# Kernel tuning notes

Hardware: AMD Instinct MI355X
Metric: run time of the kernel (lower is better)

The kernel has to match this reference:

```python
import jax, jax.numpy as jnp
import numpy as np

BATCH = 8192
DIM = 256
TEMP = 0.001
EPS = 1e-12  # torch F.normalize eps


def setup_inputs() -> dict:
    key = jax.random.key(0)
    k1, k2 = jax.random.split(key)
    proj_1 = jax.random.normal(k1, (BATCH, DIM), dtype=jnp.float32)
    proj_2 = jax.random.normal(k2, (BATCH, DIM), dtype=jnp.float32)
    return {"proj_1": proj_1, "proj_2": proj_2}


def _l2_normalize(x):
    norm = jnp.maximum(jnp.linalg.norm(x, axis=1, keepdims=True), EPS)
    return x / norm


def reference(proj_1, proj_2):
    # L2-normalize rows (SimCLR z_i, z_j)
    z_i = _l2_normalize(proj_1)  # [B, D]
    z_j = _l2_normalize(proj_2)  # [B, D]
    # cosine similarity of unit vectors == dot product -> single matmul
    sim = jnp.einsum("id,jd->ij", z_i, z_j)  # [B, B]
    positives = jnp.diagonal(sim)  # [B]
    n = positives / TEMP
    all_losses = -n + jax.scipy.special.logsumexp(sim / TEMP, axis=1)
    loss = jnp.sum(all_losses) / BATCH
    return (loss, jnp.sum(positives))
```

## Files before the change

### kernel.cpp

```cpp
#include <hip/hip_runtime.h>
#include <hip/hip_fp8.h>
#include <stdint.h>
#include <stddef.h>

#define BATCH 8192
#define DIM   256

#define LN2F 0.6931471805599453f
#define SCALE_ZJ 16.0f
#define SCALE_ZI 90.16844005556021f

typedef int   v8i    __attribute__((ext_vector_type(8)));
typedef float f32x16 __attribute__((ext_vector_type(16)));


static __device__ __forceinline__ uint8_t f2fp8(float f) {
  __hip_fp8_e4m3 q(f);
  return *reinterpret_cast<uint8_t*>(&q);
}

static __device__ __forceinline__ void stage8(const uint8_t* __restrict__ src,
                                              uint8_t* dst, int tid) {
#pragma unroll
  for (int it = 0; it < 2; ++it) {
    const int off = it * 4096 + tid * 16;
    __builtin_amdgcn_global_load_lds(
        (const __attribute__((address_space(1))) void*)(src + off),
        (__attribute__((address_space(3))) void*)(dst + off),
        16, 0, 0);
  }
}

__global__ __launch_bounds__(256) void prep_kernel(
    const float* __restrict__ p1, const float* __restrict__ p2,
    uint8_t* __restrict__ Zi8, uint8_t* __restrict__ Zj8,
    float* __restrict__ pos) {
  const int lane = threadIdx.x & 63;
  const int w    = threadIdx.x >> 6;
  const int row  = blockIdx.x * 4 + w;

  const float4 x1 = ((const float4*)p1)[row * 64 + lane];
  const float4 x2 = ((const float4*)p2)[row * 64 + lane];
  float ss1 = x1.x * x1.x + x1.y * x1.y + x1.z * x1.z + x1.w * x1.w;
  float ss2 = x2.x * x2.x + x2.y * x2.y + x2.z * x2.z + x2.w * x2.w;
  float d   = x1.x * x2.x + x1.y * x2.y + x1.z * x2.z + x1.w * x2.w;
#pragma unroll
  for (int m = 1; m < 64; m <<= 1) {
    ss1 += __shfl_xor(ss1, m);
    ss2 += __shfl_xor(ss2, m);
    d   += __shfl_xor(d, m);
  }
  const float n1 = fmaxf(sqrtf(ss1), 1e-12f);
  const float n2 = fmaxf(sqrtf(ss2), 1e-12f);
  if (lane == 0) pos[row] = d / (n1 * n2);

  const float sI = SCALE_ZI / n1;
  const float sJ = SCALE_ZJ / n2;
  uchar4 u1, u2;
  u1.x = f2fp8(x1.x * sI); u1.y = f2fp8(x1.y * sI);
  u1.z = f2fp8(x1.z * sI); u1.w = f2fp8(x1.w * sI);
  u2.x = f2fp8(x2.x * sJ); u2.y = f2fp8(x2.y * sJ);
  u2.z = f2fp8(x2.z * sJ); u2.w = f2fp8(x2.w * sJ);

  const size_t tb = (size_t)(row >> 5) * 8192;
  const int off = (lane >> 4) * 2048 + ((lane >> 2) & 1) * 1024 +
                  (((lane >> 3) & 1) * 32 + (row & 31)) * 16 + (lane & 3) * 4;
  *(uchar4*)(Zi8 + tb + off) = u1;
  *(uchar4*)(Zj8 + tb + off) = u2;
}

static __device__ __forceinline__ void lse_update(const f32x16& acc,
                                                  float& m, float& l) {
  float t0 = fmaxf(fmaxf(acc[0],  acc[1]),  acc[2]);
  float t1 = fmaxf(fmaxf(acc[3],  acc[4]),  acc[5]);
  float t2 = fmaxf(fmaxf(acc[6],  acc[7]),  acc[8]);
  float t3 = fmaxf(fmaxf(acc[9],  acc[10]), acc[11]);
  t0 = fmaxf(fmaxf(t0, t1), fmaxf(fmaxf(acc[12], acc[13]), acc[14]));
  t2 = fmaxf(fmaxf(t2, t3), acc[15]);
  const float mn = fmaxf(m, fmaxf(t0, t2));
  float s0 = 0.f, s1 = 0.f;
#pragma unroll
  for (int r = 0; r < 16; r += 2) {
    s0 += __builtin_amdgcn_exp2f(acc[r + 0] - mn);
    s1 += __builtin_amdgcn_exp2f(acc[r + 1] - mn);
  }
  l = l * __builtin_amdgcn_exp2f(m - mn) + (s0 + s1);
  m = mn;
}

__global__ __launch_bounds__(256, 3) void lse_kernel(
    const uint8_t* __restrict__ Zi8, const uint8_t* __restrict__ Zj8,
    float* __restrict__ plse) {
  const int bid   = blockIdx.x;
  const int chunk = bid & 31;
  const int rb    = bid >> 5;
  const int tid   = threadIdx.x;
  const int lane  = tid & 63;
  const int w     = tid >> 6;
  const int r32   = lane & 31;
  const int h     = lane >> 5;
  const int iBase = rb * 256 + w * 64;

  __shared__ __align__(16) uint8_t lds[4][8192];

  v8i b0[4], b1[4];
  const uint8_t* zb = Zi8 + (size_t)(rb * 8 + w * 2) * 8192 + lane * 16;
#pragma unroll
  for (int q = 0; q < 4; ++q) {
    union { int4 i4[2]; v8i v; } u0, u1;
    u0.i4[0] = *(const int4*)(zb + q * 2048);
    u0.i4[1] = *(const int4*)(zb + q * 2048 + 1024);
    u1.i4[0] = *(const int4*)(zb + 8192 + q * 2048);
    u1.i4[1] = *(const int4*)(zb + 8192 + q * 2048 + 1024);
    b0[q] = u0.v; b1[q] = u1.v;
  }
#pragma unroll
  for (int q = 0; q < 4; ++q) { asm("" : "+v"(b0[q])); asm("" : "+v"(b1[q])); }

  float m0 = -1e30f, l0 = 0.f, m1 = -1e30f, l1 = 0.f;

  const uint8_t* src = Zj8 + (size_t)chunk * (8 * 8192);

  stage8(src, &lds[0][0], tid);
  stage8(src + 8192, &lds[1][0], tid);

  for (int s = 0; s < 4; ++s) {
    __syncthreads();
    if (s < 3) {
      stage8(src + (size_t)(2 * s + 2) * 8192, &lds[(2 * s + 2) & 3][0], tid);
      stage8(src + (size_t)(2 * s + 3) * 8192, &lds[(2 * s + 3) & 3][0], tid);
    }
#pragma unroll
    for (int sub = 0; sub < 2; ++sub) {
      const uint8_t* buf = &lds[(2 * s + sub) & 3][0] + lane * 16;
      f32x16 acc0 = {}, acc1 = {};
      __builtin_amdgcn_s_setprio(1);
#pragma unroll
      for (int q = 0; q < 4; ++q) {
        union { int4 i4[2]; v8i v; } ua;
        ua.i4[0] = *(const int4*)(buf + q * 2048);
        ua.i4[1] = *(const int4*)(buf + q * 2048 + 1024);
        acc0 = __builtin_amdgcn_mfma_scale_f32_32x32x64_f8f6f4(
            ua.v, b0[q], acc0, 0, 0, 0, 0x7F7F7F7F, 0, 0x7F7F7F7F);
        acc1 = __builtin_amdgcn_mfma_scale_f32_32x32x64_f8f6f4(
            ua.v, b1[q], acc1, 0, 0, 0, 0x7F7F7F7F, 0, 0x7F7F7F7F);
      }
      __builtin_amdgcn_s_setprio(0);
      lse_update(acc0, m0, l0);
      lse_update(acc1, m1, l1);
    }
  }

#pragma unroll
  for (int p = 0; p < 2; ++p) {
    float m = p ? m1 : m0;
    float l = p ? l1 : l0;
    const float mo = __shfl_xor(m, 32);
    const float lo = __shfl_xor(l, 32);
    const float mn = fmaxf(m, mo);
    l = l * __builtin_amdgcn_exp2f(m - mn) + lo * __builtin_amdgcn_exp2f(mo - mn);
    if (h == 0) {
      const int i = iBase + p * 32 + r32;
      plse[(size_t)i * 32 + chunk] = mn + __builtin_amdgcn_logf(l);
    }
  }
}

__global__ __launch_bounds__(256) void finalize_kernel(
    const float* __restrict__ plse, const float* __restrict__ pos,
    float2* __restrict__ bpart, unsigned int* __restrict__ counter,
    float* __restrict__ out) {
  const int tid = threadIdx.x;
  const int row = blockIdx.x * 256 + tid;
  float v[32];
#pragma unroll
  for (int c = 0; c < 8; ++c) {
    const float4 q = ((const float4*)(plse + (size_t)row * 32))[c];
    v[c * 4 + 0] = q.x; v[c * 4 + 1] = q.y; v[c * 4 + 2] = q.z; v[c * 4 + 3] = q.w;
  }
  float M = v[0];
#pragma unroll
  for (int c = 1; c < 32; ++c) M = fmaxf(M, v[c]);
  float S = 0.0f;
#pragma unroll
  for (int c = 0; c < 32; ++c) S += __builtin_amdgcn_exp2f(v[c] - M);
  const float lse = LN2F * (M + __builtin_amdgcn_logf(S));
  const float pv  = pos[row];
  float lsum = lse - 1000.0f * pv;
  float psum = pv;
#pragma unroll
  for (int msk = 1; msk < 64; msk <<= 1) {
    lsum += __shfl_xor(lsum, msk);
    psum += __shfl_xor(psum, msk);
  }
  __shared__ float sl[4], sp[4];
  const int w = tid >> 6, lane = tid & 63;
  if (lane == 0) { sl[w] = lsum; sp[w] = psum; }
  __syncthreads();
  if (tid == 0) {
    union { float2 f; unsigned long long u; } pk;
    pk.f = make_float2(sl[0] + sl[1] + sl[2] + sl[3],
                       sp[0] + sp[1] + sp[2] + sp[3]);
    __hip_atomic_store((unsigned long long*)&bpart[blockIdx.x], pk.u,
                       __ATOMIC_RELEASE, __HIP_MEMORY_SCOPE_AGENT);
    const unsigned int t = __hip_atomic_fetch_add(
        counter, 1u, __ATOMIC_ACQ_REL, __HIP_MEMORY_SCOPE_AGENT);
    if (t == 31u) {
      float L = 0.f, P = 0.f;
#pragma unroll
      for (int i = 0; i < 32; ++i) {
        union { float2 f; unsigned long long u; } q2;
        q2.u = __hip_atomic_load((const unsigned long long*)&bpart[i],
                                 __ATOMIC_ACQUIRE, __HIP_MEMORY_SCOPE_AGENT);
        L += q2.f.x; P += q2.f.y;
      }
      out[0] = L / (float)BATCH;
      out[1] = P;
    }
  }
}

extern "C" void kernel_launch(void* const* d_in, const int* in_sizes, int n_in,
                              void* d_out, int out_size, void* d_ws, size_t ws_size,
                              hipStream_t stream) {
  const float* p1 = (const float*)d_in[0];
  const float* p2 = (const float*)d_in[1];
  float* out = (float*)d_out;
  uint8_t* ws = (uint8_t*)d_ws;

  uint8_t* Zi8          = ws;
  uint8_t* Zj8          = ws + (size_t)2 * 1024 * 1024;
  float* pos            = (float*)(ws + (size_t)4 * 1024 * 1024);
  float2* bpart         = (float2*)(ws + (size_t)4 * 1024 * 1024 + 32 * 1024);
  unsigned int* counter = (unsigned int*)(ws + (size_t)4 * 1024 * 1024 + 40 * 1024);
  float* plse           = (float*)(ws + (size_t)4 * 1024 * 1024 + 64 * 1024);

  hipMemsetAsync(counter, 0, sizeof(unsigned int), stream);
  prep_kernel<<<dim3(2048), dim3(256), 0, stream>>>(p1, p2, Zi8, Zj8, pos);
  lse_kernel<<<dim3(1024), dim3(256), 0, stream>>>(Zi8, Zj8, plse);
  finalize_kernel<<<dim3(32), dim3(256), 0, stream>>>(plse, pos, bpart, counter, out);
}
```

Measured before the change: 46.95 us.

## Stage whole Zj chunk in 64KB LDS with two-half prefetch instead of ring buffer

Replaces the 4-slot 8KB LDS ring buffer, which needed four barriers, with a single 64KB LDS buffer. The first half is loaded before the Zi register loads and the second half is issued after the first barrier, so only two barriers are needed. The goal is to cut synchronisation overhead and expose more load-compute overlap. The larger LDS footprint lowers occupancy, so launch bounds drop from 3 to 2 blocks per CU, which reduces latency hiding across blocks.

```diff
diff --git a/kernel.cpp b/kernel.cpp
--- a/kernel.cpp
+++ b/kernel.cpp
@@ -17,18 +17,6 @@
 static __device__ __forceinline__ uint8_t f2fp8(float f) {
   __hip_fp8_e4m3 q(f);
   return *reinterpret_cast<uint8_t*>(&q);
-}
-
-static __device__ __forceinline__ void stage8(const uint8_t* __restrict__ src,
-                                              uint8_t* dst, int tid) {
-#pragma unroll
-  for (int it = 0; it < 2; ++it) {
-    const int off = it * 4096 + tid * 16;
-    __builtin_amdgcn_global_load_lds(
-        (const __attribute__((address_space(1))) void*)(src + off),
-        (__attribute__((address_space(3))) void*)(dst + off),
-        16, 0, 0);
-  }
 }
 
 __global__ __launch_bounds__(256) void prep_kernel(
@@ -88,7 +76,7 @@
   m = mn;
 }
 
-__global__ __launch_bounds__(256, 3) void lse_kernel(
+__global__ __launch_bounds__(256, 2) void lse_kernel(
     const uint8_t* __restrict__ Zi8, const uint8_t* __restrict__ Zj8,
     float* __restrict__ plse) {
   const int bid   = blockIdx.x;
@@ -96,12 +84,22 @@
   const int rb    = bid >> 5;
   const int tid   = threadIdx.x;
   const int lane  = tid & 63;
-  const int w     = tid >> 6;
   const int r32   = lane & 31;
   const int h     = lane >> 5;
+  const int w     = tid >> 6;
   const int iBase = rb * 256 + w * 64;
 
-  __shared__ __align__(16) uint8_t lds[4][8192];
+  __shared__ __align__(16) uint8_t lds[65536];
+
+  const uint8_t* src = Zj8 + (size_t)chunk * 65536;
+
+#pragma unroll
+  for (int it = 0; it < 8; ++it) {
+    const int off = it * 4096 + tid * 16;
+    __builtin_amdgcn_global_load_lds(
+        (const __attribute__((address_space(1))) void*)(src + off),
+        (__attribute__((address_space(3))) void*)(lds + off), 16, 0, 0);
+  }
 
   v8i b0[4], b1[4];
   const uint8_t* zb = Zi8 + (size_t)(rb * 8 + w * 2) * 8192 + lane * 16;
@@ -119,20 +117,23 @@
 
   float m0 = -1e30f, l0 = 0.f, m1 = -1e30f, l1 = 0.f;
 
-  const uint8_t* src = Zj8 + (size_t)chunk * (8 * 8192);
-
-  stage8(src, &lds[0][0], tid);
-  stage8(src + 8192, &lds[1][0], tid);
-
-  for (int s = 0; s < 4; ++s) {
-    __syncthreads();
-    if (s < 3) {
-      stage8(src + (size_t)(2 * s + 2) * 8192, &lds[(2 * s + 2) & 3][0], tid);
-      stage8(src + (size_t)(2 * s + 3) * 8192, &lds[(2 * s + 3) & 3][0], tid);
-    }
-#pragma unroll
-    for (int sub = 0; sub < 2; ++sub) {
-      const uint8_t* buf = &lds[(2 * s + sub) & 3][0] + lane * 16;
+  __syncthreads();
+
+#pragma unroll
+  for (int it = 8; it < 16; ++it) {
+    const int off = it * 4096 + tid * 16;
+    __builtin_amdgcn_global_load_lds(
+        (const __attribute__((address_space(1))) void*)(src + off),
+        (__attribute__((address_space(3))) void*)(lds + off), 16, 0, 0);
+  }
+  asm volatile("" ::: "memory");
+
+#pragma unroll
+  for (int half = 0; half < 2; ++half) {
+    if (half == 1) __syncthreads();
+#pragma unroll
+    for (int t = 0; t < 4; ++t) {
+      const uint8_t* buf = lds + (half * 4 + t) * 8192 + lane * 16;
       f32x16 acc0 = {}, acc1 = {};
       __builtin_amdgcn_s_setprio(1);
 #pragma unroll
```

Result: no change. 46.79 us (-0.3%).
